# Kernel optimization log

Measured on AMD Instinct MI355X. Metric: run time of the kernel, lower is better.

The kernel has to match this reference:

```python
import jax, jax.numpy as jnp
import numpy as np

B, T, C, H = 4, 4096, 1024, 64

def setup_inputs() -> dict:
    key = jax.random.key(0)
    k1, k2, k3, k4, k5 = jax.random.split(key, 5)
    scale = 0.02
    return {
        "x": jax.random.normal(k1, (B, T, C), dtype=jnp.float32),
        "head_bias": jax.random.normal(k2, (T, T), dtype=jnp.float32) * 0.1,
        "w_k": jax.random.normal(k3, (C, H), dtype=jnp.float32) * scale,
        "w_q": jax.random.normal(k4, (C, H), dtype=jnp.float32) * scale,
        "w_v": jax.random.normal(k5, (C, H), dtype=jnp.float32) * scale,
    }

def reference(x, head_bias, w_k, w_q, w_v):
    # x: (B,T,C) ; projections: (B,T,H)
    k = jnp.einsum('btc,ch->bth', x, w_k)
    q = jnp.einsum('btc,ch->bth', x, w_q)
    v = jnp.einsum('btc,ch->bth', x, w_v)
    Tq = x.shape[1]
    # scores: (B,T,T) with RPE bias and causal mask
    scores = jnp.einsum('bqh,bkh->bqk', q, k) * (k.shape[-1] ** -0.5)
    scores = scores + head_bias[None, :, :]
    causal = jnp.tril(jnp.ones((Tq, Tq), dtype=bool))
    scores = jnp.where(causal[None, :, :], scores, -jnp.inf)
    weights = jax.nn.softmax(scores, axis=-1)
    out = jnp.einsum('bqk,bkh->bqh', weights, v)
    return out
```

## Files before the change

kernel.cpp:

```cpp
#include <hip/hip_runtime.h>
#include <hip/hip_bf16.h>


#define T_DIM 4096
#define C_DIM 1024
#define CK    256

typedef __attribute__((ext_vector_type(8))) short s16x8;
typedef __attribute__((ext_vector_type(4))) float f32x4;
typedef __attribute__((ext_vector_type(2))) unsigned int u32x2;

__device__ __forceinline__ short f2bf(float f) {
    unsigned u = __builtin_bit_cast(unsigned, f);
    u += 0x7FFFu + ((u >> 16) & 1u);
    return (short)(u >> 16);
}
__device__ __forceinline__ unsigned pack2(float a, float b) {
    unsigned ua = __builtin_bit_cast(unsigned, a);
    unsigned ub = __builtin_bit_cast(unsigned, b);
    ua += 0x7FFFu + ((ua >> 16) & 1u);
    ub += 0x7FFFu + ((ub >> 16) & 1u);
    return __builtin_amdgcn_perm(ub, ua, 0x07060302u);
}
__device__ __forceinline__ float bf2f(short s) {
    unsigned u = ((unsigned)(unsigned short)s) << 16;
    return __builtin_bit_cast(float, u);
}
__device__ __forceinline__ int chunk_off(int qt) {
    int g = qt >> 4, r = qt & 15;
    return qt + 8 * g * (g - 1) + r * g;
}

__global__ __launch_bounds__(256) void prep_frag(
    const float* __restrict__ wk, const float* __restrict__ wq,
    const float* __restrict__ wv, short* __restrict__ wfrag)
{
    int ksAll = blockIdx.x, mat = blockIdx.y;
    const float* w = (mat == 0) ? wk : ((mat == 1) ? wq : wv);
    float sc = (mat == 1) ? 0.125f : 1.0f;
    int nt = threadIdx.x >> 6, lane = threadIdx.x & 63;
    int quad = lane >> 4, l15 = lane & 15;
    int h = nt * 16 + l15;
    int cb = ksAll * 32 + quad * 8;
    s16x8 v;
    #pragma unroll
    for (int j = 0; j < 8; ++j) v[j] = f2bf(w[(cb + j) * 64 + h] * sc);
    *(s16x8*)&wfrag[((ksAll * 12 + mat * 4 + nt) * 64 + lane) * 8] = v;
}

union ProjSmem {
    short xs[32][1032];
    struct {
        short comb[2][16][136];
        short vsep[64][40];
    } c;
};

__global__ __launch_bounds__(256, 2) void proj_fused(
    const float* __restrict__ x, const short* __restrict__ wfrag,
    short* __restrict__ qb, short* __restrict__ kfrag, short* __restrict__ vfrag)
{
    __shared__ __align__(16) ProjSmem sm;

    int tid = threadIdx.x;
    int w = tid >> 6, lane = tid & 63;
    int rt = w >> 1, h = w & 1;
    int l15 = lane & 15, quad = lane >> 4;
    int m0 = blockIdx.x * 32;

    s16x8 fA[12], fB[12];
    {
        const s16x8* fb = (const s16x8*)&wfrag[((size_t)(h * 16) * 12 * 64 + lane) * 8];
        #pragma unroll
        for (int f = 0; f < 12; ++f) fA[f] = fb[f * 64];
    }

    #pragma unroll 8
    for (int p = 0; p < 32; ++p) {
        f32x4 v = *(const f32x4*)&x[(size_t)(m0 + p) * C_DIM + tid * 4];
        u32x2 d;
        d[0] = pack2(v[0], v[1]);
        d[1] = pack2(v[2], v[3]);
        *(u32x2*)&sm.xs[p][tid * 4] = d;
    }
    __syncthreads();

    f32x4 acc[12];
    #pragma unroll
    for (int i = 0; i < 12; ++i) acc[i] = (f32x4){0.f, 0.f, 0.f, 0.f};

    #pragma unroll 1
    for (int ks = 0; ks < 16; ks += 2) {
        {
            const s16x8* fb = (const s16x8*)&wfrag[((size_t)(h * 16 + ks + 1) * 12 * 64 + lane) * 8];
            #pragma unroll
            for (int f = 0; f < 12; ++f) fB[f] = fb[f * 64];
        }
        s16x8 af = *(const s16x8*)&sm.xs[rt * 16 + l15][(h * 16 + ks) * 32 + quad * 8];
        #pragma unroll
        for (int f = 0; f < 12; ++f)
            acc[f] = __builtin_amdgcn_mfma_f32_16x16x32_bf16(af, fA[f], acc[f], 0, 0, 0);
        if (ks + 2 < 16) {
            const s16x8* fb = (const s16x8*)&wfrag[((size_t)(h * 16 + ks + 2) * 12 * 64 + lane) * 8];
            #pragma unroll
            for (int f = 0; f < 12; ++f) fA[f] = fb[f * 64];
        }
        s16x8 af2 = *(const s16x8*)&sm.xs[rt * 16 + l15][(h * 16 + ks + 1) * 32 + quad * 8];
        #pragma unroll
        for (int f = 0; f < 12; ++f)
            acc[f] = __builtin_amdgcn_mfma_f32_16x16x32_bf16(af2, fB[f], acc[f], 0, 0, 0);
    }
    __syncthreads();

    if (h == 1) {
        #pragma unroll
        for (int f = 0; f < 8; ++f)
            #pragma unroll
            for (int r = 0; r < 4; ++r)
                sm.c.comb[rt][quad * 4 + r][(f >> 2) * 64 + (f & 3) * 16 + l15] = f2bf(acc[f][r]);
        #pragma unroll
        for (int f = 8; f < 12; ++f)
            #pragma unroll
            for (int r = 0; r < 4; ++r)
                sm.c.vsep[(f & 3) * 16 + l15][rt * 16 + quad * 4 + r] = f2bf(acc[f][r]);
    }
    __syncthreads();
    if (h == 0) {
        #pragma unroll
        for (int f = 0; f < 8; ++f)
            #pragma unroll
            for (int r = 0; r < 4; ++r) {
                int col = (f >> 2) * 64 + (f & 3) * 16 + l15, rr = quad * 4 + r;
                sm.c.comb[rt][rr][col] = f2bf(acc[f][r] + bf2f(sm.c.comb[rt][rr][col]));
            }
        #pragma unroll
        for (int f = 8; f < 12; ++f)
            #pragma unroll
            for (int r = 0; r < 4; ++r) {
                int hh = (f & 3) * 16 + l15, kk = rt * 16 + quad * 4 + r;
                sm.c.vsep[hh][kk] = f2bf(acc[f][r] + bf2f(sm.c.vsep[hh][kk]));
            }
    }
    __syncthreads();

    int b = m0 >> 12, t0 = m0 & 4095;
    int t016 = t0 >> 4, kt32 = t0 >> 5;
    {
        int row = tid >> 3, ch = tid & 7;
        s16x8 v = *(const s16x8*)&sm.c.comb[row >> 4][row & 15][64 + ch * 8];
        *(s16x8*)&qb[(size_t)(m0 + row) * 64 + ch * 8] = v;
    }
    {
        int kt = w & 1, ks = w >> 1;
        s16x8 v = *(const s16x8*)&sm.c.comb[kt][l15][ks * 32 + quad * 8];
        *(s16x8*)&kfrag[(size_t)(((b * 256 + t016 + kt) * 2 + ks) * 64 + lane) * 8] = v;
    }
    {
        int nt = w;
        s16x8 v = *(const s16x8*)&sm.c.vsep[nt * 16 + l15][quad * 8];
        *(s16x8*)&vfrag[(size_t)(((b * 128 + kt32) * 4 + nt) * 64 + lane) * 8] = v;
    }
}

#define LOADK(AK, k0) do {                                                    \
    int _kt16 = (k0) >> 4;                                                    \
    _Pragma("unroll")                                                         \
    for (int _n = 0; _n < 2; ++_n) {                                          \
        const short* _kp = kfb + (size_t)((_kt16 + _n) * 2) * 512 + lane * 8; \
        AK[_n * 2]     = *(const s16x8*)_kp;                                  \
        AK[_n * 2 + 1] = *(const s16x8*)(_kp + 512);                          \
    }                                                                         \
} while (0)

#define COMPUTEK(AK, k0) do {                                                 \
    int _kt32 = (k0) >> 5;                                                    \
    int _kl = (k0) - kstart;                                                  \
    s16x8 _bv[4];                                                             \
    _Pragma("unroll")                                                         \
    for (int _n = 0; _n < 4; ++_n)                                            \
        _bv[_n] = *(const s16x8*)(vfb + (size_t)(_kt32 * 4 + _n) * 512 + lane * 8); \
    f32x4 _aS[2];                                                             \
    _Pragma("unroll")                                                         \
    for (int _n = 0; _n < 2; ++_n) {                                          \
        _aS[_n] = (f32x4){0.f, 0.f, 0.f, 0.f};                                \
        _aS[_n] = __builtin_amdgcn_mfma_f32_16x16x32_bf16(AK[_n*2],   aq0, _aS[_n], 0, 0, 0); \
        _aS[_n] = __builtin_amdgcn_mfma_f32_16x16x32_bf16(AK[_n*2+1], aq1, _aS[_n], 0, 0, 0); \
    }                                                                         \
    _Pragma("unroll")                                                         \
    for (int _n = 0; _n < 2; ++_n) {                                          \
        f32x4 _vb = *(const f32x4*)&blds[l15][_kl + _n * 16 + quad * 4];      \
        float _sv[4];                                                         \
        _Pragma("unroll")                                                     \
        for (int _r = 0; _r < 4; ++_r) {                                      \
            _sv[_r] = _aS[_n][_r] + _vb[_r];                                  \
            if (mask_on && ((k0) + _n * 16 + quad * 4 + _r > strip0 + l15))   \
                _sv[_r] = -__builtin_inff();                                  \
            float _p = __expf(_sv[_r]);                                       \
            _sv[_r] = _p;                                                     \
            l_sum += _p;                                                      \
        }                                                                     \
        u32x2 _d;                                                             \
        _d[0] = pack2(_sv[0], _sv[1]);                                        \
        _d[1] = pack2(_sv[2], _sv[3]);                                        \
        *(u32x2*)&plds[w][l15][_n * 16 + quad * 4] = _d;                      \
    }                                                                         \
    s16x8 _ap = *(const s16x8*)&plds[w][l15][quad * 8];                       \
    _Pragma("unroll")                                                         \
    for (int _n = 0; _n < 4; ++_n)                                            \
        accO[_n] = __builtin_amdgcn_mfma_f32_16x16x32_bf16(_ap, _bv[_n], accO[_n], 0, 0, 0); \
} while (0)

__global__ __launch_bounds__(256, 4) void flash_part(
    const short* __restrict__ qb, const short* __restrict__ kfrag,
    const short* __restrict__ vfrag, const float* __restrict__ bias,
    short* __restrict__ po)
{
    int qt = blockIdx.x, c = blockIdx.y;
    if (c > (qt >> 4)) return;
    int q0 = qt * 16;
    int kstart = c * CK;
    int kend = min(kstart + CK, q0 + 16);

    __shared__ __align__(16) float blds[16][260];
    __shared__ __align__(16) short plds[4][16][40];

    int w = threadIdx.x >> 6, lane = threadIdx.x & 63;
    int b = w;
    int l15 = lane & 15, quad = lane >> 4;
    int strip0 = q0;

    #pragma unroll
    for (int p = 0; p < 4; ++p)
        *(f32x4*)&blds[p * 4 + w][lane * 4] =
            *(const f32x4*)&bias[(size_t)(q0 + p * 4 + w) * T_DIM + kstart + lane * 4];

    const short* qrow = qb + (size_t)(b * T_DIM + strip0 + l15) * 64;
    s16x8 aq0 = *(const s16x8*)(qrow + quad * 8);
    s16x8 aq1 = *(const s16x8*)(qrow + 32 + quad * 8);

    float l_sum = 0.f;
    f32x4 accO[4];
    #pragma unroll
    for (int nt = 0; nt < 4; ++nt) accO[nt] = (f32x4){0.f, 0.f, 0.f, 0.f};

    const short* kfb = kfrag + (size_t)b * 256 * 2 * 512;
    const short* vfb = vfrag + (size_t)b * 128 * 4 * 512;
    bool mask_on = (kend > strip0);

    __syncthreads();

    s16x8 akA[4], akB[4];
    int k0 = kstart;
    LOADK(akA, k0);
    while (true) {
        int k1 = k0 + 32;
        bool more = (k1 < kend);
        if (more) LOADK(akB, k1);
        COMPUTEK(akA, k0);
        if (!more) break;
        k0 = k1; k1 = k0 + 32;
        bool more2 = (k1 < kend);
        if (more2) LOADK(akA, k1);
        COMPUTEK(akB, k0);
        if (!more2) break;
        k0 = k1;
    }

    l_sum += __shfl_xor(l_sum, 16, 64);
    l_sum += __shfl_xor(l_sum, 32, 64);

    short* base = po + (size_t)((chunk_off(qt) + c) * 4 + b) * 1040;
    #pragma unroll
    for (int nt = 0; nt < 4; ++nt)
        #pragma unroll
        for (int r = 0; r < 4; ++r)
            base[(quad * 4 + r) * 64 + nt * 16 + l15] = f2bf(accO[nt][r]);
    if (quad == 0) base[1024 + l15] = f2bf(l_sum);
}

__global__ __launch_bounds__(256) void flash_reduce(
    const short* __restrict__ po, float* __restrict__ out)
{
    int idx = blockIdx.x * 256 + threadIdx.x;
    int row = idx >> 3, c8 = idx & 7;
    int b = row >> 12, t = row & 4095;
    int qt = t >> 4, rloc = t & 15;
    int nc = (t >> 8) + 1;
    int off = chunk_off(qt);
    float o[8];
    #pragma unroll
    for (int j = 0; j < 8; ++j) o[j] = 0.f;
    float l = 0.f;
    #pragma unroll 1
    for (int cc = 0; cc < nc; ++cc) {
        const short* base = po + (size_t)((off + cc) * 4 + b) * 1040;
        s16x8 v = *(const s16x8*)&base[rloc * 64 + c8 * 8];
        #pragma unroll
        for (int j = 0; j < 8; ++j) o[j] += bf2f(v[j]);
        l += bf2f(base[1024 + rloc]);
    }
    float inv = 1.0f / l;
    f32x4 r0 = (f32x4){o[0] * inv, o[1] * inv, o[2] * inv, o[3] * inv};
    f32x4 r1 = (f32x4){o[4] * inv, o[5] * inv, o[6] * inv, o[7] * inv};
    float* op = &out[(size_t)row * 64 + c8 * 8];
    *(f32x4*)op = r0;
    *(f32x4*)(op + 4) = r1;
}

extern "C" void kernel_launch(void* const* d_in, const int* in_sizes, int n_in,
                              void* d_out, int out_size, void* d_ws, size_t ws_size,
                              hipStream_t stream) {
    (void)in_sizes; (void)n_in; (void)out_size; (void)ws_size;
    const float* x    = (const float*)d_in[0];
    const float* bias = (const float*)d_in[1];
    const float* wk   = (const float*)d_in[2];
    const float* wq   = (const float*)d_in[3];
    const float* wv   = (const float*)d_in[4];
    float* out = (float*)d_out;

    short* wfrag = (short*)d_ws;
    short* qb    = wfrag + 196608;
    short* kfrag = qb + 1048576;
    short* vfrag = kfrag + 1048576;
    short* po    = vfrag + 1048576;

    prep_frag<<<dim3(32, 3), dim3(256), 0, stream>>>(wk, wq, wv, wfrag);
    proj_fused<<<dim3(512), dim3(256), 0, stream>>>(x, wfrag, qb, kfrag, vfrag);
    flash_part<<<dim3(256, 16), dim3(256), 0, stream>>>(qb, kfrag, vfrag, bias, po);
    flash_reduce<<<dim3(512), dim3(256), 0, stream>>>(po, out);
}
```

Before: 195.1 us.

## Share K/V chunk across 8 query tiles via async LDS staging in flash_part

flash_part blocks used to map one query tile to four waves, one per batch, and each wave streamed its own K fragments from global memory. Now each 512-thread block covers one batch and eight consecutive query tiles, one per wave. The block stages the 256-key K and V chunk into LDS once with global_load_lds, so all eight waves reuse it. Bias is now read per lane straight from global into registers and prefetched one step ahead, replacing the LDS bias tile. This cuts global K/V traffic, but raises LDS use per block and makes waves in a block do uneven work near the causal diagonal.

```diff
diff --git a/kernel.cpp b/kernel.cpp
--- a/kernel.cpp
+++ b/kernel.cpp
@@ -29,6 +29,11 @@
 __device__ __forceinline__ int chunk_off(int qt) {
     int g = qt >> 4, r = qt & 15;
     return qt + 8 * g * (g - 1) + r * g;
+}
+__device__ __forceinline__ void async16(const short* g, short* l) {
+    __builtin_amdgcn_global_load_lds(
+        (const __attribute__((address_space(1))) unsigned int*)g,
+        (__attribute__((address_space(3))) unsigned int*)l, 16, 0, 0);
 }
 
 __global__ __launch_bounds__(256) void prep_frag(
@@ -162,108 +167,122 @@
     }
 }
 
-#define LOADK(AK, k0) do {                                                    \
-    int _kt16 = (k0) >> 4;                                                    \
+#define SOFT(N, AS, BV) do {                                                  \
+    float _sv[4];                                                             \
     _Pragma("unroll")                                                         \
-    for (int _n = 0; _n < 2; ++_n) {                                          \
-        const short* _kp = kfb + (size_t)((_kt16 + _n) * 2) * 512 + lane * 8; \
-        AK[_n * 2]     = *(const s16x8*)_kp;                                  \
-        AK[_n * 2 + 1] = *(const s16x8*)(_kp + 512);                          \
+    for (int _r = 0; _r < 4; ++_r) {                                          \
+        _sv[_r] = (AS)[_r] + (BV)[_r];                                        \
+        if (mask_on && (kabs + (N) * 16 + quad * 4 + _r > q0 + l15))          \
+            _sv[_r] = -__builtin_inff();                                      \
+        float _p = __expf(_sv[_r]);                                           \
+        _sv[_r] = _p;                                                         \
+        l_sum += _p;                                                          \
     }                                                                         \
+    u32x2 _d;                                                                 \
+    _d[0] = pack2(_sv[0], _sv[1]);                                            \
+    _d[1] = pack2(_sv[2], _sv[3]);                                            \
+    *(u32x2*)&plds[w][l15][(N) * 16 + quad * 4] = _d;                         \
 } while (0)
 
-#define COMPUTEK(AK, k0) do {                                                 \
-    int _kt32 = (k0) >> 5;                                                    \
-    int _kl = (k0) - kstart;                                                  \
-    s16x8 _bv[4];                                                             \
-    _Pragma("unroll")                                                         \
-    for (int _n = 0; _n < 4; ++_n)                                            \
-        _bv[_n] = *(const s16x8*)(vfb + (size_t)(_kt32 * 4 + _n) * 512 + lane * 8); \
-    f32x4 _aS[2];                                                             \
-    _Pragma("unroll")                                                         \
-    for (int _n = 0; _n < 2; ++_n) {                                          \
-        _aS[_n] = (f32x4){0.f, 0.f, 0.f, 0.f};                                \
-        _aS[_n] = __builtin_amdgcn_mfma_f32_16x16x32_bf16(AK[_n*2],   aq0, _aS[_n], 0, 0, 0); \
-        _aS[_n] = __builtin_amdgcn_mfma_f32_16x16x32_bf16(AK[_n*2+1], aq1, _aS[_n], 0, 0, 0); \
-    }                                                                         \
-    _Pragma("unroll")                                                         \
-    for (int _n = 0; _n < 2; ++_n) {                                          \
-        f32x4 _vb = *(const f32x4*)&blds[l15][_kl + _n * 16 + quad * 4];      \
-        float _sv[4];                                                         \
-        _Pragma("unroll")                                                     \
-        for (int _r = 0; _r < 4; ++_r) {                                      \
-            _sv[_r] = _aS[_n][_r] + _vb[_r];                                  \
-            if (mask_on && ((k0) + _n * 16 + quad * 4 + _r > strip0 + l15))   \
-                _sv[_r] = -__builtin_inff();                                  \
-            float _p = __expf(_sv[_r]);                                       \
-            _sv[_r] = _p;                                                     \
-            l_sum += _p;                                                      \
-        }                                                                     \
-        u32x2 _d;                                                             \
-        _d[0] = pack2(_sv[0], _sv[1]);                                        \
-        _d[1] = pack2(_sv[2], _sv[3]);                                        \
-        *(u32x2*)&plds[w][l15][_n * 16 + quad * 4] = _d;                      \
-    }                                                                         \
+#define COMPUTEK(KREL, B0, B1) do {                                           \
+    int _kt16 = (KREL) >> 4;                                                  \
+    int _kt32 = (KREL) >> 5;                                                  \
+    int kabs = kstart + (KREL);                                               \
+    s16x8 _ak0 = *(const s16x8*)&klds[(_kt16 * 2 + 0) * 512 + lane * 8];      \
+    s16x8 _ak1 = *(const s16x8*)&klds[(_kt16 * 2 + 1) * 512 + lane * 8];      \
+    s16x8 _ak2 = *(const s16x8*)&klds[(_kt16 * 2 + 2) * 512 + lane * 8];      \
+    s16x8 _ak3 = *(const s16x8*)&klds[(_kt16 * 2 + 3) * 512 + lane * 8];      \
+    s16x8 _bv0 = *(const s16x8*)&vlds[(_kt32 * 4 + 0) * 512 + lane * 8];      \
+    s16x8 _bv1 = *(const s16x8*)&vlds[(_kt32 * 4 + 1) * 512 + lane * 8];      \
+    s16x8 _bv2 = *(const s16x8*)&vlds[(_kt32 * 4 + 2) * 512 + lane * 8];      \
+    s16x8 _bv3 = *(const s16x8*)&vlds[(_kt32 * 4 + 3) * 512 + lane * 8];      \
+    f32x4 _aS0 = (f32x4){0.f, 0.f, 0.f, 0.f};                                 \
+    f32x4 _aS1 = (f32x4){0.f, 0.f, 0.f, 0.f};                                 \
+    _aS0 = __builtin_amdgcn_mfma_f32_16x16x32_bf16(_ak0, aq0, _aS0, 0, 0, 0); \
+    _aS0 = __builtin_amdgcn_mfma_f32_16x16x32_bf16(_ak1, aq1, _aS0, 0, 0, 0); \
+    _aS1 = __builtin_amdgcn_mfma_f32_16x16x32_bf16(_ak2, aq0, _aS1, 0, 0, 0); \
+    _aS1 = __builtin_amdgcn_mfma_f32_16x16x32_bf16(_ak3, aq1, _aS1, 0, 0, 0); \
+    SOFT(0, _aS0, B0);                                                        \
+    SOFT(1, _aS1, B1);                                                        \
     s16x8 _ap = *(const s16x8*)&plds[w][l15][quad * 8];                       \
-    _Pragma("unroll")                                                         \
-    for (int _n = 0; _n < 4; ++_n)                                            \
-        accO[_n] = __builtin_amdgcn_mfma_f32_16x16x32_bf16(_ap, _bv[_n], accO[_n], 0, 0, 0); \
+    accO[0] = __builtin_amdgcn_mfma_f32_16x16x32_bf16(_ap, _bv0, accO[0], 0, 0, 0); \
+    accO[1] = __builtin_amdgcn_mfma_f32_16x16x32_bf16(_ap, _bv1, accO[1], 0, 0, 0); \
+    accO[2] = __builtin_amdgcn_mfma_f32_16x16x32_bf16(_ap, _bv2, accO[2], 0, 0, 0); \
+    accO[3] = __builtin_amdgcn_mfma_f32_16x16x32_bf16(_ap, _bv3, accO[3], 0, 0, 0); \
 } while (0)
 
-__global__ __launch_bounds__(256, 4) void flash_part(
+__global__ __launch_bounds__(512, 4) void flash_part(
     const short* __restrict__ qb, const short* __restrict__ kfrag,
     const short* __restrict__ vfrag, const float* __restrict__ bias,
     short* __restrict__ po)
 {
-    int qt = blockIdx.x, c = blockIdx.y;
-    if (c > (qt >> 4)) return;
+    int g = blockIdx.x;
+    int c = blockIdx.y;
+    int b = blockIdx.z;
+    if (c > (g >> 1)) return;
+
+    __shared__ __align__(16) short klds[32 * 512];
+    __shared__ __align__(16) short vlds[32 * 512];
+    __shared__ __align__(16) short plds[8][16][40];
+
+    int tid = threadIdx.x;
+    int w = tid >> 6, lane = tid & 63;
+    int l15 = lane & 15, quad = lane >> 4;
+
+    int qt = g * 8 + w;
     int q0 = qt * 16;
     int kstart = c * CK;
     int kend = min(kstart + CK, q0 + 16);
-
-    __shared__ __align__(16) float blds[16][260];
-    __shared__ __align__(16) short plds[4][16][40];
-
-    int w = threadIdx.x >> 6, lane = threadIdx.x & 63;
-    int b = w;
-    int l15 = lane & 15, quad = lane >> 4;
-    int strip0 = q0;
-
-    #pragma unroll
-    for (int p = 0; p < 4; ++p)
-        *(f32x4*)&blds[p * 4 + w][lane * 4] =
-            *(const f32x4*)&bias[(size_t)(q0 + p * 4 + w) * T_DIM + kstart + lane * 4];
-
-    const short* qrow = qb + (size_t)(b * T_DIM + strip0 + l15) * 64;
+    int nk = kend - kstart;
+    bool mask_on = (kend > q0);
+
+    const short* ksrc = kfrag + (size_t)((b * 256 + c * 16) * 2) * 512;
+    const short* vsrc = vfrag + (size_t)((b * 128 + c * 8) * 4) * 512;
+    #pragma unroll
+    for (int i = 0; i < 4; ++i) {
+        int seg = i * 8 + w;
+        async16(ksrc + (size_t)seg * 512 + lane * 8, &klds[seg * 512]);
+    }
+    #pragma unroll
+    for (int i = 0; i < 4; ++i) {
+        int seg = i * 8 + w;
+        async16(vsrc + (size_t)seg * 512 + lane * 8, &vlds[seg * 512]);
+    }
+
+    const short* qrow = qb + (size_t)(b * T_DIM + q0 + l15) * 64;
     s16x8 aq0 = *(const s16x8*)(qrow + quad * 8);
     s16x8 aq1 = *(const s16x8*)(qrow + 32 + quad * 8);
+    const float* brow = bias + (size_t)(q0 + l15) * T_DIM + kstart;
+    f32x4 bA0 = *(const f32x4*)&brow[quad * 4];
+    f32x4 bA1 = *(const f32x4*)&brow[16 + quad * 4];
+    f32x4 bB0, bB1;
 
     float l_sum = 0.f;
     f32x4 accO[4];
     #pragma unroll
     for (int nt = 0; nt < 4; ++nt) accO[nt] = (f32x4){0.f, 0.f, 0.f, 0.f};
 
-    const short* kfb = kfrag + (size_t)b * 256 * 2 * 512;
-    const short* vfb = vfrag + (size_t)b * 128 * 4 * 512;
-    bool mask_on = (kend > strip0);
-
-    __syncthreads();
-
-    s16x8 akA[4], akB[4];
-    int k0 = kstart;
-    LOADK(akA, k0);
+    __syncthreads();
+
+    int krel = 0;
     while (true) {
-        int k1 = k0 + 32;
-        bool more = (k1 < kend);
-        if (more) LOADK(akB, k1);
-        COMPUTEK(akA, k0);
+        int kn = krel + 32;
+        bool more = (kn < nk);
+        if (more) {
+            bB0 = *(const f32x4*)&brow[kn + quad * 4];
+            bB1 = *(const f32x4*)&brow[kn + 16 + quad * 4];
+        }
+        COMPUTEK(krel, bA0, bA1);
         if (!more) break;
-        k0 = k1; k1 = k0 + 32;
-        bool more2 = (k1 < kend);
-        if (more2) LOADK(akA, k1);
-        COMPUTEK(akB, k0);
+        krel = kn; kn = krel + 32;
+        bool more2 = (kn < nk);
+        if (more2) {
+            bA0 = *(const f32x4*)&brow[kn + quad * 4];
+            bA1 = *(const f32x4*)&brow[kn + 16 + quad * 4];
+        }
+        COMPUTEK(krel, bB0, bB1);
         if (!more2) break;
-        k0 = k1;
+        krel = kn;
     }
 
     l_sum += __shfl_xor(l_sum, 16, 64);
@@ -326,6 +345,6 @@
 
     prep_frag<<<dim3(32, 3), dim3(256), 0, stream>>>(wk, wq, wv, wfrag);
     proj_fused<<<dim3(512), dim3(256), 0, stream>>>(x, wfrag, qb, kfrag, vfrag);
-    flash_part<<<dim3(256, 16), dim3(256), 0, stream>>>(qb, kfrag, vfrag, bias, po);
+    flash_part<<<dim3(32, 16, 4), dim3(512), 0, stream>>>(qb, kfrag, vfrag, bias, po);
     flash_reduce<<<dim3(512), dim3(256), 0, stream>>>(po, out);
 }
```

After: 204.5 us. 4.8% more time.

## Transpose P fragment in registers via permlane swaps and prefetch V fragments

Applied to the files above, without the earlier changes.

The per-wave LDS staging buffer used to convert the softmax probabilities from the QK^T MFMA output layout into the PV MFMA A-operand layout is removed. The layout change is now done in registers with v_permlane32_swap/v_permlane16_swap instructions. V fragments are also double-buffered and loaded one iteration ahead, like the K fragments. This drops the LDS write/read round trip and its latency from the inner loop, at the cost of more VGPRs under the 4-wave occupancy bound, and relies on the permlane mapping matching the MFMA operand layout.

```diff
diff --git a/kernel.cpp b/kernel.cpp
--- a/kernel.cpp
+++ b/kernel.cpp
@@ -9,6 +9,7 @@
 typedef __attribute__((ext_vector_type(8))) short s16x8;
 typedef __attribute__((ext_vector_type(4))) float f32x4;
 typedef __attribute__((ext_vector_type(2))) unsigned int u32x2;
+typedef __attribute__((ext_vector_type(4))) unsigned int u32x4;
 
 __device__ __forceinline__ short f2bf(float f) {
     unsigned u = __builtin_bit_cast(unsigned, f);
@@ -172,42 +173,51 @@
     }                                                                         \
 } while (0)
 
-#define COMPUTEK(AK, k0) do {                                                 \
+#define LOADV(BV, k0) do {                                                    \
     int _kt32 = (k0) >> 5;                                                    \
-    int _kl = (k0) - kstart;                                                  \
-    s16x8 _bv[4];                                                             \
     _Pragma("unroll")                                                         \
     for (int _n = 0; _n < 4; ++_n)                                            \
-        _bv[_n] = *(const s16x8*)(vfb + (size_t)(_kt32 * 4 + _n) * 512 + lane * 8); \
-    f32x4 _aS[2];                                                             \
+        BV[_n] = *(const s16x8*)(vfb + (size_t)(_kt32 * 4 + _n) * 512 + lane * 8); \
+} while (0)
+
+#define SOFT(N, AS, KL, PLO, PHI) do {                                        \
+    f32x4 _vb = *(const f32x4*)&blds[l15][(KL) + (N) * 16 + quad * 4];        \
+    float _sv[4];                                                             \
     _Pragma("unroll")                                                         \
-    for (int _n = 0; _n < 2; ++_n) {                                          \
-        _aS[_n] = (f32x4){0.f, 0.f, 0.f, 0.f};                                \
-        _aS[_n] = __builtin_amdgcn_mfma_f32_16x16x32_bf16(AK[_n*2],   aq0, _aS[_n], 0, 0, 0); \
-        _aS[_n] = __builtin_amdgcn_mfma_f32_16x16x32_bf16(AK[_n*2+1], aq1, _aS[_n], 0, 0, 0); \
+    for (int _r = 0; _r < 4; ++_r) {                                          \
+        _sv[_r] = (AS)[_r] + _vb[_r];                                         \
+        if (mask_on && (kabs + (N) * 16 + quad * 4 + _r > strip0 + l15))      \
+            _sv[_r] = -__builtin_inff();                                      \
+        float _p = __expf(_sv[_r]);                                           \
+        _sv[_r] = _p;                                                         \
+        l_sum += _p;                                                          \
     }                                                                         \
-    _Pragma("unroll")                                                         \
-    for (int _n = 0; _n < 2; ++_n) {                                          \
-        f32x4 _vb = *(const f32x4*)&blds[l15][_kl + _n * 16 + quad * 4];      \
-        float _sv[4];                                                         \
-        _Pragma("unroll")                                                     \
-        for (int _r = 0; _r < 4; ++_r) {                                      \
-            _sv[_r] = _aS[_n][_r] + _vb[_r];                                  \
-            if (mask_on && ((k0) + _n * 16 + quad * 4 + _r > strip0 + l15))   \
-                _sv[_r] = -__builtin_inff();                                  \
-            float _p = __expf(_sv[_r]);                                       \
-            _sv[_r] = _p;                                                     \
-            l_sum += _p;                                                      \
-        }                                                                     \
-        u32x2 _d;                                                             \
-        _d[0] = pack2(_sv[0], _sv[1]);                                        \
-        _d[1] = pack2(_sv[2], _sv[3]);                                        \
-        *(u32x2*)&plds[w][l15][_n * 16 + quad * 4] = _d;                      \
-    }                                                                         \
-    s16x8 _ap = *(const s16x8*)&plds[w][l15][quad * 8];                       \
-    _Pragma("unroll")                                                         \
-    for (int _n = 0; _n < 4; ++_n)                                            \
-        accO[_n] = __builtin_amdgcn_mfma_f32_16x16x32_bf16(_ap, _bv[_n], accO[_n], 0, 0, 0); \
+    PLO = pack2(_sv[0], _sv[1]);                                              \
+    PHI = pack2(_sv[2], _sv[3]);                                              \
+} while (0)
+
+#define COMPUTEK(AK, BV, k0) do {                                             \
+    int _kl = (k0) - kstart;                                                  \
+    int kabs = (k0);                                                          \
+    f32x4 _aS0 = (f32x4){0.f, 0.f, 0.f, 0.f};                                 \
+    f32x4 _aS1 = (f32x4){0.f, 0.f, 0.f, 0.f};                                 \
+    _aS0 = __builtin_amdgcn_mfma_f32_16x16x32_bf16(AK[0], aq0, _aS0, 0, 0, 0); \
+    _aS0 = __builtin_amdgcn_mfma_f32_16x16x32_bf16(AK[1], aq1, _aS0, 0, 0, 0); \
+    _aS1 = __builtin_amdgcn_mfma_f32_16x16x32_bf16(AK[2], aq0, _aS1, 0, 0, 0); \
+    _aS1 = __builtin_amdgcn_mfma_f32_16x16x32_bf16(AK[3], aq1, _aS1, 0, 0, 0); \
+    unsigned _p0, _p1, _p2, _p3;                                              \
+    SOFT(0, _aS0, _kl, _p0, _p1);                                             \
+    SOFT(1, _aS1, _kl, _p2, _p3);                                             \
+    asm("v_permlane32_swap_b32 %0, %1" : "+v"(_p0), "+v"(_p2));               \
+    asm("v_permlane16_swap_b32 %0, %1" : "+v"(_p0), "+v"(_p2));               \
+    asm("v_permlane32_swap_b32 %0, %1" : "+v"(_p1), "+v"(_p3));               \
+    asm("v_permlane16_swap_b32 %0, %1" : "+v"(_p1), "+v"(_p3));               \
+    u32x4 _apu = (u32x4){_p0, _p1, _p2, _p3};                                 \
+    s16x8 _ap = __builtin_bit_cast(s16x8, _apu);                              \
+    accO[0] = __builtin_amdgcn_mfma_f32_16x16x32_bf16(_ap, BV[0], accO[0], 0, 0, 0); \
+    accO[1] = __builtin_amdgcn_mfma_f32_16x16x32_bf16(_ap, BV[1], accO[1], 0, 0, 0); \
+    accO[2] = __builtin_amdgcn_mfma_f32_16x16x32_bf16(_ap, BV[2], accO[2], 0, 0, 0); \
+    accO[3] = __builtin_amdgcn_mfma_f32_16x16x32_bf16(_ap, BV[3], accO[3], 0, 0, 0); \
 } while (0)
 
 __global__ __launch_bounds__(256, 4) void flash_part(
@@ -222,7 +232,6 @@
     int kend = min(kstart + CK, q0 + 16);
 
     __shared__ __align__(16) float blds[16][260];
-    __shared__ __align__(16) short plds[4][16][40];
 
     int w = threadIdx.x >> 6, lane = threadIdx.x & 63;
     int b = w;
@@ -249,19 +258,20 @@
 
     __syncthreads();
 
-    s16x8 akA[4], akB[4];
+    s16x8 akA[4], akB[4], bvA[4], bvB[4];
     int k0 = kstart;
     LOADK(akA, k0);
+    LOADV(bvA, k0);
     while (true) {
         int k1 = k0 + 32;
         bool more = (k1 < kend);
-        if (more) LOADK(akB, k1);
-        COMPUTEK(akA, k0);
+        if (more) { LOADK(akB, k1); LOADV(bvB, k1); }
+        COMPUTEK(akA, bvA, k0);
         if (!more) break;
         k0 = k1; k1 = k0 + 32;
         bool more2 = (k1 < kend);
-        if (more2) LOADK(akA, k1);
-        COMPUTEK(akB, k0);
+        if (more2) { LOADK(akA, k1); LOADV(bvA, k1); }
+        COMPUTEK(akB, bvB, k0);
         if (!more2) break;
         k0 = k1;
     }
```

After: 195.6 us. About the same (+0.3%).
